# Kernel tuning notes

Measured on AMD Instinct MI355X. Metric: run time of the kernel, lower is better.

## Reference

```python
import jax, jax.numpy as jnp
import numpy as np

# dims
N, D, H = 10000, 512, 8            # nodes, node hidden, heads
E, EL, M = 120000, 60000, 600000   # graph edges, local edges, line-graph edges
ED, EH = 64, 8                     # edge feat dim (relation_share_heads), edge heads
L, R = 4, 100                      # gnn layers, relation vocab
DK, EDK = D // H, ED // EH
SCALE_N, SCALE_E = float(np.sqrt(DK)), float(np.sqrt(EDK))


def layer_norm(h, g, b, eps=1e-5):
    mu = jnp.mean(h, axis=-1, keepdims=True)
    var = jnp.mean((h - mu) ** 2, axis=-1, keepdims=True)
    return (h - mu) * jax.lax.rsqrt(var + eps) * g + b


def setup_inputs() -> dict:
    key = jax.random.key(0)
    ks = iter(jax.random.split(key, 80))

    def nrm(shape, s=0.02):
        return jax.random.normal(next(ks), shape, jnp.float32) * s

    inp = {
        "x": jax.random.normal(next(ks), (N, D), jnp.float32),
        "rel_embed": nrm((R, ED), 1.0),
        # node-update (RAT) params, stacked over layers
        "Wq": nrm((L, D, D)), "bq": jnp.zeros((L, D), jnp.float32),
        "Wk": nrm((L, D, D)), "Wv": nrm((L, D, D)),
        "Wo": nrm((L, D, D)), "bo": jnp.zeros((L, D), jnp.float32),
        "ln1_g": jnp.ones((L, D), jnp.float32), "ln1_b": jnp.zeros((L, D), jnp.float32),
        "F1": nrm((L, D, 4 * D)), "f1b": jnp.zeros((L, 4 * D), jnp.float32),
        "F2": nrm((L, 4 * D, D)), "f2b": jnp.zeros((L, D), jnp.float32),
        "ln2_g": jnp.ones((L, D), jnp.float32), "ln2_b": jnp.zeros((L, D), jnp.float32),
        # edge-update (metapath line-graph attention) params
        "Eq": nrm((L, ED, ED)), "eqb": jnp.zeros((L, ED), jnp.float32),
        "Ek": nrm((L, ED, ED)), "Ev": nrm((L, ED, ED)),
        "Eo": nrm((L, ED, ED)), "eob": jnp.zeros((L, ED), jnp.float32),
        "Ns": nrm((L, D, ED)), "nsb": jnp.zeros((L, ED), jnp.float32),
        "Nd": nrm((L, D, ED)), "ndb": jnp.zeros((L, ED), jnp.float32),
        "eln1_g": jnp.ones((L, ED), jnp.float32), "eln1_b": jnp.zeros((L, ED), jnp.float32),
        "G1": nrm((L, ED, 4 * ED)), "g1b": jnp.zeros((L, 4 * ED), jnp.float32),
        "G2": nrm((L, 4 * ED, ED)), "g2b": jnp.zeros((L, ED), jnp.float32),
        "eln2_g": jnp.ones((L, ED), jnp.float32), "eln2_b": jnp.zeros((L, ED), jnp.float32),
        # graph structure (constants)
        "edge_feat": jax.random.randint(next(ks), (E,), 0, R),
        "local_index": jnp.arange(EL),
        "src_ids": jax.random.randint(next(ks), (EL,), 0, N),
        "dst_ids": jax.random.randint(next(ks), (EL,), 0, N),
        "g_src": jax.random.randint(next(ks), (E,), 0, N),
        "g_dst": jax.random.randint(next(ks), (E,), 0, N),
        "lg_src": jax.random.randint(next(ks), (M,), 0, EL),
        "lg_dst": jax.random.randint(next(ks), (M,), 0, EL),
    }
    return inp


def reference(x, rel_embed, Wq, bq, Wk, Wv, Wo, bo, ln1_g, ln1_b, F1, f1b, F2, f2b,
              ln2_g, ln2_b, Eq, eqb, Ek, Ev, Eo, eob, Ns, nsb, Nd, ndb,
              eln1_g, eln1_b, G1, g1b, G2, g2b, eln2_g, eln2_b,
              edge_feat, local_index, src_ids, dst_ids, g_src, g_dst, lg_src, lg_dst):
    lg_x = rel_embed[edge_feat]        # [E, ED] relation embedding gather
    lg_x_local = lg_x[local_index]     # [EL, ED]
    for i in range(L):
        x_in = x
        # ---- node update: relation-aware multi-head attention over g ----
        q = (x_in @ Wq[i] + bq[i]).reshape(N, H, DK)
        k = (x_in @ Wk[i]).reshape(N, H, DK)
        v = (x_in @ Wv[i]).reshape(N, H, DK)
        e = lg_x[:, None, :]           # relation feat shared across heads (edim == d_k)
        ks = k[g_src] + e              # [E, H, DK]
        vs = v[g_src] + e
        s = jnp.einsum('ehd,ehd->eh', ks, q[g_dst]) / SCALE_N
        w = jnp.exp(jnp.clip(s, -10.0, 10.0))
        wv = jax.ops.segment_sum(w[..., None] * vs, g_dst, num_segments=N)
        z = jax.ops.segment_sum(w, g_dst, num_segments=N)
        o = (wv / jnp.maximum(z, 1e-9)[..., None]).reshape(N, D)
        h = layer_norm(x_in + o @ Wo[i] + bo[i], ln1_g[i], ln1_b[i])
        x = layer_norm(h + jax.nn.relu(h @ F1[i] + f1b[i]) @ F2[i] + f2b[i], ln2_g[i], ln2_b[i])
        # ---- edge update: attention over line graph lg, metapath = shared node feat ----
        src_x = x_in[src_ids]          # index_select on pre-update x
        dst_x = x_in[dst_ids]
        qe = (lg_x_local @ Eq[i] + eqb[i] + src_x @ Ns[i] + nsb[i]).reshape(EL, EH, EDK)
        me = (dst_x @ Nd[i] + ndb[i]).reshape(EL, EH, EDK)
        ke = (lg_x_local @ Ek[i]).reshape(EL, EH, EDK) + me
        ve = (lg_x_local @ Ev[i]).reshape(EL, EH, EDK) + me
        se = jnp.einsum('mhd,mhd->mh', ke[lg_src], qe[lg_dst]) / SCALE_E
        we = jnp.exp(jnp.clip(se, -10.0, 10.0))
        wve = jax.ops.segment_sum(we[..., None] * ve[lg_src], lg_dst, num_segments=EL)
        ze = jax.ops.segment_sum(we, lg_dst, num_segments=EL)
        oe = (wve / jnp.maximum(ze, 1e-9)[..., None]).reshape(EL, ED)
        he = layer_norm(lg_x_local + oe @ Eo[i] + eob[i], eln1_g[i], eln1_b[i])
        out_local = layer_norm(he + jax.nn.relu(he @ G1[i] + g1b[i]) @ G2[i] + g2b[i],
                               eln2_g[i], eln2_b[i])
        lg_x = lg_x.at[local_index].set(out_local)   # masked_scatter_
        lg_x_local = out_local
    return (x, lg_x_local)
```

## Files before the change

kernel.cpp:

```cpp
#include <hip/hip_runtime.h>
#include <math.h>

#define NN   10000
#define DD   512
#define NH   8
#define NE   120000
#define NEL  60000
#define NLG  600000
#define ED   64
#define NEH  8
#define NL   4
#define QKVW 1536

typedef __attribute__((ext_vector_type(8))) short bf16x8;
typedef __attribute__((ext_vector_type(8))) unsigned short u16x8;
typedef __attribute__((ext_vector_type(4))) float f32x4;

__device__ __forceinline__ unsigned short f2b(float f) {
    union { float f; unsigned u; } c; c.f = f;
    unsigned u = c.u;
    unsigned r = u + 0x7FFFu + ((u >> 16) & 1u);
    return (unsigned short)(r >> 16);
}
__device__ __forceinline__ float b2f(unsigned short b) {
// ... 88 lines not shown

static __global__ __launch_bounds__(256)
void hist2_k(const int* __restrict__ gdst, const int* __restrict__ ldst,
             int* __restrict__ gcnt, int* __restrict__ ecnt) {
    int i = blockIdx.x * 256 + threadIdx.x;
    if (i < NE) atomicAdd(&gcnt[gdst[i]], 1);
    else if (i < NE + NLG) atomicAdd(&ecnt[ldst[i - NE]], 1);
}

static __global__ __launch_bounds__(256)
void scanA2_k(const int* __restrict__ gcnt, const int* __restrict__ ecnt,
              int* __restrict__ goff, int* __restrict__ eoff,
              int* __restrict__ bsum, int nbG) {
    __shared__ int sm[256];
    const int t = threadIdx.x;
    const bool isG = blockIdx.x < (unsigned)nbG;
    const int b = isG ? blockIdx.x : blockIdx.x - nbG;
    const int n = isG ? NN : NEL;
    const int* cnt = isG ? gcnt : ecnt;
    int* off = isG ? goff : eoff;
    int* bs = bsum + (isG ? 0 : 512);
    const int i = b * 256 + t;
    int v = (i < n) ? cnt[i] : 0;
    sm[t] = v; __syncthreads();
    int x = v;
    #pragma unroll
    for (int d = 1; d < 256; d <<= 1) {
        int y = (t >= d) ? sm[t - d] : 0;
        __syncthreads();
        x += y; sm[t] = x; __syncthreads();
    }
    if (i < n) off[i] = x - v;
    if (t == 255) bs[b] = x;
}

static __global__ __launch_bounds__(1024)
void scanB2_k(int* __restrict__ bsum, int nbG, int nbE) {
    __shared__ int sm[1024];
    const int t = threadIdx.x;
    int* bs = bsum + (blockIdx.x ? 512 : 0);
    const int nb = blockIdx.x ? nbE : nbG;
    int v = (t < nb) ? bs[t] : 0;
    sm[t] = v; __syncthreads();
    int x = v;
    #pragma unroll
    for (int d = 1; d < 1024; d <<= 1) {
        int y = (t >= d) ? sm[t - d] : 0;
        __syncthreads();
        x += y; sm[t] = x; __syncthreads();
    }
    if (t < nb) bs[t] = x - v;
}

static __global__ __launch_bounds__(256)
void scanC2_k(const int* __restrict__ bsum, int* __restrict__ goff,
              int* __restrict__ eoff, int* __restrict__ gcur,
              int* __restrict__ ecur, int nbG) {
    const bool isG = blockIdx.x < (unsigned)nbG;
    const int b = isG ? blockIdx.x : blockIdx.x - nbG;
    const int n = isG ? NN : NEL;
    int* off = isG ? goff : eoff;
    int* cur = isG ? gcur : ecur;
    const int* bs = bsum + (isG ? 0 : 512);
    int i = b * 256 + threadIdx.x;
    if (i < n) { int o = off[i] + bs[b]; off[i] = o; cur[i] = o; }
}

static __global__ __launch_bounds__(256)
void scatterpack_k(const int* __restrict__ gdst, const int* __restrict__ ldst,
                   const int* __restrict__ gsrc, const int* __restrict__ lsrc,
                   int* __restrict__ gcur, int* __restrict__ ecur,
                   int2* __restrict__ npack, int* __restrict__ esrc) {
    int i = blockIdx.x * 256 + threadIdx.x;
    if (i < NE) {
        int p = atomicAdd(&gcur[gdst[i]], 1);
        npack[p] = make_int2(i, gsrc[i]);
    } else if (i < NE + NLG) {
        int k = i - NE;
        int p = atomicAdd(&ecur[ldst[k]], 1);
        esrc[p] = lsrc[k];
    }
}

static __global__ __launch_bounds__(256)
void gemm_bf16_k(const unsigned short* __restrict__ A,
                 const unsigned short* __restrict__ A2, const int* __restrict__ idx2,
                 const unsigned short* __restrict__ Bt, const float* __restrict__ bias,
                 const float* __restrict__ addC, const unsigned short* __restrict__ addCb,
                 float* __restrict__ C, unsigned short* __restrict__ Cb,
                 int M, int K, int Nc, int doRelu, int K1)
{
    __shared__ unsigned short Asl[64 * 64];
    __shared__ unsigned short Bsl[64 * 64];
    const int tid  = threadIdx.x;
    const int lane = tid & 63;
    const int wave = tid >> 6;
    const int wr = (wave >> 1) * 32;
    const int wc = (wave & 1) * 32;

    const int nwg = gridDim.x * gridDim.y;
    const int hw = blockIdx.y * gridDim.x + blockIdx.x;
    const int q8 = nwg >> 3, r8 = nwg & 7;
    const int xcd = hw & 7, rest = hw >> 3;
    const int logical = (xcd < r8 ? xcd * (q8 + 1) : r8 * (q8 + 1) + (xcd - r8) * q8) + rest;
    const int bm = (logical / gridDim.x) * 64;
    const int bn = (logical % gridDim.x) * 64;

    const int rl8 = lane >> 3;
    const int sl8 = lane & 7;
    int ga[2]; long ia[2]; bool av[2]; int acw[2];
    int gb[2]; int bcw[2];
    #pragma unroll
    for (int c = 0; c < 2; ++c) {
        int ar = wave * 16 + c * 8 + rl8;
        ga[c] = bm + ar;
        av[c] = ga[c] < M;
        ia[c] = (A2 && av[c]) ? (long)idx2[ga[c]] : 0;
        acw[c] = (sl8 ^ (ar & 7)) * 8;
        int br = wave * 16 + c * 8 + rl8;
        gb[c] = bn + br;
        bcw[c] = (sl8 ^ (br & 7)) * 8;
    }

    auto stage = [&](int k0) {
        #pragma unroll
        for (int c = 0; c < 2; ++c) {
            const unsigned short* s;
            if (!A2)            s = A  + (long)ga[c] * K  + k0 + acw[c];
            else if (k0 < K1)   s = A  + (long)ga[c] * K1 + k0 + acw[c];
            else                s = A2 + ia[c] * DD + (k0 - K1) + acw[c];
            if (av[c]) gl16(s, Asl + (wave * 16 + c * 8) * 64);
            gl16(Bt + (long)gb[c] * K + k0 + bcw[c], Bsl + (wave * 16 + c * 8) * 64);
        }
    };

    f32x4 acc[2][2] = {};
    const int rbase = lane & 15;
    const int ks = lane >> 4;

    for (int k0 = 0; k0 < K; k0 += 64) {
        stage(k0);
        __syncthreads();
        #pragma unroll
        for (int h = 0; h < 2; ++h) {
            bf16x8 af[2], bfr[2];
            #pragma unroll
            for (int mi = 0; mi < 2; ++mi) {
                int r = wr + mi * 16 + rbase;
                int p = (h * 4 + ks) ^ (r & 7);
                af[mi] = *reinterpret_cast<const bf16x8*>(Asl + r * 64 + p * 8);
            }
            #pragma unroll
            for (int ni = 0; ni < 2; ++ni) {
                int r = wc + ni * 16 + rbase;
                int p = (h * 4 + ks) ^ (r & 7);
                bfr[ni] = *reinterpret_cast<const bf16x8*>(Bsl + r * 64 + p * 8);
            }
            #pragma unroll
            for (int mi = 0; mi < 2; ++mi)
                #pragma unroll
                for (int ni = 0; ni < 2; ++ni)
                    acc[mi][ni] = __builtin_amdgcn_mfma_f32_16x16x32_bf16(
                        af[mi], bfr[ni], acc[mi][ni], 0, 0, 0);
        }
        __syncthreads();
    }

    const int colBase = bn + wc + rbase;
    const int rowBase = bm + wr + ks * 4;
    #pragma unroll
    for (int mi = 0; mi < 2; ++mi) {
        #pragma unroll
        for (int j = 0; j < 4; ++j) {
            int r = rowBase + mi * 16 + j;
            if (r >= M) continue;
            long ro = (long)r * Nc;
            #pragma unroll
            for (int ni = 0; ni < 2; ++ni) {
                int cc = colBase + ni * 16;
                if (cc >= Nc) continue;
                float v = acc[mi][ni][j];
                if (bias)  v += bias[cc];
                if (doRelu) v = fmaxf(v, 0.0f);
                if (addC)  v += addC[ro + cc];
                else if (addCb) v += b2f(addCb[ro + cc]);
                if (Cb) Cb[ro + cc] = f2b(v);
                else    C[ro + cc] = v;
            }
        }
    }
}

static __global__ __launch_bounds__(256)
void ln_k(const float* __restrict__ in, const unsigned short* __restrict__ inb,
          const float* __restrict__ g, const float* __restrict__ b,
          float* __restrict__ out, int Dw, int nrows,
          unsigned short* __restrict__ outb,
          unsigned short* __restrict__ out2b, const int* __restrict__ idx2)
{
    const int row = blockIdx.x * 4 + (threadIdx.x >> 6);
    if (row >= nrows) return;
    const int lane = threadIdx.x & 63;
    const int per = Dw >> 6;
    float v[8];
    float s = 0.f;
    if (inb) {
        const unsigned short* rp = inb + (long)row * Dw;
        for (int i = 0; i < per; ++i) { v[i] = b2f(rp[i * 64 + lane]); s += v[i]; }
    } else {
        const float* rp = in + (long)row * Dw;
        for (int i = 0; i < per; ++i) { v[i] = rp[i * 64 + lane]; s += v[i]; }
    }
    #pragma unroll
    for (int off = 32; off; off >>= 1) s += __shfl_xor(s, off, 64);
    const float mu = s / (float)Dw;
    float var = 0.f;
    for (int i = 0; i < per; ++i) { float d = v[i] - mu; var += d * d; }
    #pragma unroll
    for (int off = 32; off; off >>= 1) var += __shfl_xor(var, off, 64);
    const float rstd = rsqrtf(var / (float)Dw + 1e-5f);
    for (int i = 0; i < per; ++i) {
        int c = i * 64 + lane;
        float o = (v[i] - mu) * rstd * g[c] + b[c];
        if (out)   out[(long)row * Dw + c] = o;
        if (outb)  outb[(long)row * Dw + c] = f2b(o);
        if (out2b) out2b[(long)idx2[row] * Dw + c] = f2b(o);
    }
}

static __global__ __launch_bounds__(256)
void node_attn_csr_k(const unsigned short* __restrict__ qkv,
                     const unsigned short* __restrict__ lgb,
                     const int* __restrict__ goff, const int2* __restrict__ npack,
                     unsigned short* __restrict__ ob)
{
    int node = blockIdx.x * 4 + (threadIdx.x >> 6);
    if (node >= NN) return;
    const int lane = threadIdx.x & 63;
    float qv[8];
    {
        u16x8 q8 = *reinterpret_cast<const u16x8*>(qkv + (long)node * QKVW + lane * 8);
        #pragma unroll
        for (int i = 0; i < 8; ++i) qv[i] = b2f(q8[i]);
    }
    float wva[8] = {0.f, 0.f, 0.f, 0.f, 0.f, 0.f, 0.f, 0.f};
    float zac = 0.f;
    int j = goff[node];
    const int hi = (node + 1 < NN) ? goff[node + 1] : NE;
    const int eoffl = (lane & 7) * 8;

    for (; j + 2 <= hi; j += 2) {
        int2 pa = npack[j], pb = npack[j + 1];
        u16x8 kA = *reinterpret_cast<const u16x8*>(qkv + (long)pa.y * QKVW + 512 + lane * 8);
        u16x8 vA = *reinterpret_cast<const u16x8*>(qkv + (long)pa.y * QKVW + 1024 + lane * 8);
        u16x8 eA = *reinterpret_cast<const u16x8*>(lgb + (long)pa.x * ED + eoffl);
        u16x8 kB = *reinterpret_cast<const u16x8*>(qkv + (long)pb.y * QKVW + 512 + lane * 8);
        u16x8 vB = *reinterpret_cast<const u16x8*>(qkv + (long)pb.y * QKVW + 1024 + lane * 8);
        u16x8 eB = *reinterpret_cast<const u16x8*>(lgb + (long)pb.x * ED + eoffl);
        float edA[8], vvA[8], edB[8], vvB[8];
        float pA = 0.f, pB = 0.f;
        #pragma unroll
        for (int i = 0; i < 8; ++i) {
            edA[i] = b2f(eA[i]); vvA[i] = b2f(vA[i]);
            pA = fmaf(b2f(kA[i]) + edA[i], qv[i], pA);
            edB[i] = b2f(eB[i]); vvB[i] = b2f(vB[i]);
            pB = fmaf(b2f(kB[i]) + edB[i], qv[i], pB);
        }
        pA += __shfl_xor(pA, 1, 64); pA += __shfl_xor(pA, 2, 64); pA += __shfl_xor(pA, 4, 64);
        pB += __shfl_xor(pB, 1, 64); pB += __shfl_xor(pB, 2, 64); pB += __shfl_xor(pB, 4, 64);
        float wA = expf(fminf(fmaxf(pA * 0.125f, -10.0f), 10.0f));
        float wB = expf(fminf(fmaxf(pB * 0.125f, -10.0f), 10.0f));
        #pragma unroll
        for (int i = 0; i < 8; ++i) {
            wva[i] = fmaf(wA, vvA[i] + edA[i], wva[i]);
            wva[i] = fmaf(wB, vvB[i] + edB[i], wva[i]);
        }
        zac += wA + wB;
    }
    for (; j < hi; ++j) {
        int2 pa = npack[j];
        u16x8 kA = *reinterpret_cast<const u16x8*>(qkv + (long)pa.y * QKVW + 512 + lane * 8);
        u16x8 vA = *reinterpret_cast<const u16x8*>(qkv + (long)pa.y * QKVW + 1024 + lane * 8);
        u16x8 eA = *reinterpret_cast<const u16x8*>(lgb + (long)pa.x * ED + eoffl);
        float edA[8], vvA[8];
        float pA = 0.f;
        #pragma unroll
        for (int i = 0; i < 8; ++i) {
            edA[i] = b2f(eA[i]); vvA[i] = b2f(vA[i]);
            pA = fmaf(b2f(kA[i]) + edA[i], qv[i], pA);
        }
        pA += __shfl_xor(pA, 1, 64); pA += __shfl_xor(pA, 2, 64); pA += __shfl_xor(pA, 4, 64);
        float wA = expf(fminf(fmaxf(pA * 0.125f, -10.0f), 10.0f));
        #pragma unroll
        for (int i = 0; i < 8; ++i) wva[i] = fmaf(wA, vvA[i] + edA[i], wva[i]);
        zac += wA;
    }
    const float inv = 1.0f / fmaxf(zac, 1e-9f);
    u16x8 o8;
    #pragma unroll
    for (int i = 0; i < 8; ++i) o8[i] = f2b(wva[i] * inv);
    *reinterpret_cast<u16x8*>(ob + (long)node * DD + lane * 8) = o8;
}

static __global__ __launch_bounds__(256)
void lg_attn_csr_k(const unsigned short* __restrict__ qeb,
                   const unsigned short* __restrict__ keve,
                   const int* __restrict__ eoff, const int* __restrict__ esrc,
                   unsigned short* __restrict__ oeb)
{
    int d = blockIdx.x * 4 + (threadIdx.x >> 6);
    if (d >= NEL) return;
    const int lane = threadIdx.x & 63;
    const int he = lane & 7;
    const int ee = lane >> 3;
    const int hd = lane >> 3;
    float qv8[8];
    {
        u16x8 q8 = *reinterpret_cast<const u16x8*>(qeb + (long)d * ED + he * 8);
        #pragma unroll
        for (int i = 0; i < 8; ++i) qv8[i] = b2f(q8[i]);
    }
    const float qvd = b2f(qeb[(long)d * ED + lane]);
    float oa = 0.f, zac = 0.f;
    int j = eoff[d];
    const int hi = (d + 1 < NEL) ? eoff[d + 1] : NLG;

    for (; j + 8 <= hi; j += 8) {
        int sMine = esrc[j + ee];
        u16x8 k8 = *reinterpret_cast<const u16x8*>(keve + (long)sMine * 128 + he * 8);
        float p = 0.f;
        #pragma unroll
        for (int i = 0; i < 8; ++i) p = fmaf(b2f(k8[i]), qv8[i], p);
        float w = expf(fminf(fmaxf(p * 0.35355339059327373f, -10.0f), 10.0f));
        #pragma unroll
        for (int u = 0; u < 8; ++u) {
            float wu = __shfl(w, u * 8 + hd, 64);
            int   su = esrc[j + u];
            float vv = b2f(keve[(long)su * 128 + 64 + lane]);
            oa = fmaf(wu, vv, oa);
            zac += wu;
        }
    }
    for (; j < hi; ++j) {
        int s = esrc[j];
        float kv = b2f(keve[(long)s * 128 + lane]);
        float vv = b2f(keve[(long)s * 128 + 64 + lane]);
        float p = kv * qvd;
        p += __shfl_xor(p, 1, 64); p += __shfl_xor(p, 2, 64); p += __shfl_xor(p, 4, 64);
        float w = expf(fminf(fmaxf(p * 0.35355339059327373f, -10.0f), 10.0f));
        oa = fmaf(w, vv, oa);
        zac += w;
    }
    oeb[(long)d * ED + lane] = f2b(oa / fmaxf(zac, 1e-9f));
}

static inline void run_gemm(hipStream_t st, const unsigned short* A,
                            const unsigned short* Bt, const float* bias,
                            const float* addC, const unsigned short* addCb,
                            float* C, unsigned short* Cb,
                            int M, int K, int Nc, int relu)
{
    dim3 g((Nc + 63) / 64, (M + 63) / 64);
    gemm_bf16_k<<<g, 256, 0, st>>>(A, nullptr, nullptr, Bt, bias, addC, addCb,
                                   C, Cb, M, K, Nc, relu, 0);
}
static inline void run_gemm2(hipStream_t st, const unsigned short* A1,
                             const unsigned short* A2, const int* idx2,
                             const unsigned short* Bt, const float* bias,
                             unsigned short* Cb, int M, int K, int Nc, int K1)
{
    dim3 g((Nc + 63) / 64, (M + 63) / 64);
    gemm_bf16_k<<<g, 256, 0, st>>>(A1, A2, idx2, Bt, bias, nullptr, nullptr,
                                   nullptr, Cb, M, K, Nc, 0, K1);
}

extern "C" void kernel_launch(void* const* d_in, const int* in_sizes, int n_in,
                              void* d_out, int out_size, void* d_ws, size_t ws_size,
                              hipStream_t stream)
{
    const float* x_in  = (const float*)d_in[0];
    const float* rel   = (const float*)d_in[1];
    const float* Wq    = (const float*)d_in[2];
    const float* bq    = (const float*)d_in[3];
    const float* Wk    = (const float*)d_in[4];
    const float* Wv    = (const float*)d_in[5];
    const float* Wo    = (const float*)d_in[6];
    const float* bo    = (const float*)d_in[7];
    const float* ln1g  = (const float*)d_in[8];
    const float* ln1b  = (const float*)d_in[9];
    const float* F1    = (const float*)d_in[10];
    const float* f1b   = (const float*)d_in[11];
    const float* F2    = (const float*)d_in[12];
    const float* f2b_  = (const float*)d_in[13];
    const float* ln2g  = (const float*)d_in[14];
    const float* ln2b  = (const float*)d_in[15];
    const float* Eq    = (const float*)d_in[16];
    const float* eqb   = (const float*)d_in[17];
    const float* Ek    = (const float*)d_in[18];
    const float* Ev    = (const float*)d_in[19];
    const float* Eo    = (const float*)d_in[20];
    const float* eob   = (const float*)d_in[21];
    const float* Ns    = (const float*)d_in[22];
    const float* nsb   = (const float*)d_in[23];
    const float* Nd    = (const float*)d_in[24];
    const float* ndb   = (const float*)d_in[25];
    const float* eln1g = (const float*)d_in[26];
    const float* eln1b = (const float*)d_in[27];
    const float* G1    = (const float*)d_in[28];
    const float* g1b   = (const float*)d_in[29];
    const float* G2    = (const float*)d_in[30];
    const float* g2b   = (const float*)d_in[31];
    const float* eln2g = (const float*)d_in[32];
    const float* eln2b = (const float*)d_in[33];
    const int* edge_feat   = (const int*)d_in[34];
    const int* local_index = (const int*)d_in[35];
    const int* src_ids     = (const int*)d_in[36];
    const int* dst_ids     = (const int*)d_in[37];
    const int* g_src       = (const int*)d_in[38];
    const int* g_dst       = (const int*)d_in[39];
    const int* lg_src      = (const int*)d_in[40];
    const int* lg_dst      = (const int*)d_in[41];

    float* xbuf = (float*)d_out;
    float* el   = xbuf + (size_t)NN * DD;

    float* W = (float*)d_ws;
    size_t off = 0;
    auto alloc = [&](size_t n) { float* p = W + off; off += (n + 63) & ~(size_t)63; return p; };
    float* qkvb = alloc((size_t)NL * QKVW);
    float* kvb  = alloc((size_t)NL * 128);
    float* qb2  = alloc((size_t)NL * ED);

    unsigned short* bp = (unsigned short*)(W + off);
    size_t boff = 0;
    auto balloc = [&](size_t n) { unsigned short* p = bp + boff; boff += (n + 63) & ~(size_t)63; return p; };
    unsigned short* lgb = balloc((size_t)NE * ED);
    unsigned short* xb  = balloc((size_t)NN * DD);
    unsigned short* qkv = balloc((size_t)NN * QKVW);
    unsigned short* elb = balloc((size_t)NEL * ED);
    unsigned short* e1b = balloc((size_t)NEL * ED);
    unsigned short* heb = balloc((size_t)NEL * ED);
    unsigned short* qeb = balloc((size_t)NEL * ED);
    unsigned short* fgb = balloc((size_t)NN * 4 * DD);
    unsigned short* t0b = balloc((size_t)NN * DD);
    unsigned short* t2b = balloc((size_t)NEL * ED);
    unsigned short* t3b = balloc((size_t)NEL * ED);
    unsigned short* xpb = balloc((size_t)NN * DD);
    unsigned short* hb   = qkv;
    unsigned short* keve = qkv + (size_t)NN * DD;
    unsigned short* ob   = fgb;
    unsigned short* WqkvT = balloc((size_t)NL * QKVW * DD);
    unsigned short* WoT  = balloc((size_t)NL * DD * DD);
    unsigned short* F1T  = balloc((size_t)NL * DD * 4 * DD);
    unsigned short* F2T  = balloc((size_t)NL * 4 * DD * DD);
    unsigned short* KVET = balloc((size_t)NL * 128 * 576);
    unsigned short* QET  = balloc((size_t)NL * 64 * 576);
    unsigned short* EoT  = balloc((size_t)NL * ED * ED);
    unsigned short* G1T  = balloc((size_t)NL * ED * 4 * ED);
    unsigned short* G2T  = balloc((size_t)NL * 4 * ED * ED);
    int* ip = (int*)(bp + ((boff + 63) & ~(size_t)63));
    size_t ioff = 0;
    auto ialloc = [&](size_t n) { int* p = ip + ioff; ioff += (n + 63) & ~(size_t)63; return p; };
    int* gcnt = ialloc(NN);
    int* goff = ialloc(NN);
    int* gcur = ialloc(NN);
    int2* npack = (int2*)ialloc(2 * (size_t)NE);
    int* ecnt = ialloc(NEL);
    int* eoff = ialloc(NEL);
    int* ecur = ialloc(NEL);
    int* esrc = ialloc(NLG);
    int* bsum = ialloc(1024);

    TT tt;
    int bc = 0, si = 0;
    auto seg = [&](const float* src, unsigned short* dst, int K, int N,
                   long lstride, int rowStride, int rowOff, int colOff) {
        tt.src[si] = src; tt.dst[si] = dst; tt.lstride[si] = lstride;
        tt.K[si] = K; tt.Nn[si] = N; tt.rowStride[si] = rowStride;
        tt.rowOff[si] = rowOff; tt.colOff[si] = colOff;
        tt.blkStart[si] = bc;
        bc += (K / 32) * (N / 32) * NL;
        ++si;
    };
    seg(Wq, WqkvT, 512, 512, (long)QKVW * DD, DD, 0, 0);
    seg(Wk, WqkvT, 512, 512, (long)QKVW * DD, DD, 512, 0);
    seg(Wv, WqkvT, 512, 512, (long)QKVW * DD, DD, 1024, 0);
    seg(Wo, WoT, 512, 512, (long)DD * DD, DD, 0, 0);
    seg(F1, F1T, 512, 2048, (long)DD * 4 * DD, DD, 0, 0);
    seg(F2, F2T, 2048, 512, (long)4 * DD * DD, 4 * DD, 0, 0);
    seg(Ek, KVET, 64, 64, (long)128 * 576, 576, 0, 0);
    seg(Nd, KVET, 512, 64, (long)128 * 576, 576, 0, 64);
    seg(Ev, KVET, 64, 64, (long)128 * 576, 576, 64, 0);
    seg(Nd, KVET, 512, 64, (long)128 * 576, 576, 64, 64);
    seg(Eq, QET, 64, 64, (long)64 * 576, 576, 0, 0);
    seg(Ns, QET, 512, 64, (long)64 * 576, 576, 0, 64);
    seg(Eo, EoT, 64, 64, (long)ED * ED, ED, 0, 0);
    seg(G1, G1T, 64, 256, (long)ED * 4 * ED, ED, 0, 0);
    seg(G2, G2T, 256, 64, (long)4 * ED * ED, 4 * ED, 0, 0);
    ttrans_all_k<<<bc, 256, 0, stream>>>(tt);
    biases_k<<<(NL * QKVW + 255) / 256, 256, 0, stream>>>(bq, ndb, eqb, nsb, qkvb, kvb, qb2);

    const int nbG = (NN + 255) / 256, nbE = (NEL + 255) / 256;
    zero2_k<<<nbE, 256, 0, stream>>>(gcnt, ecnt);
    hist2_k<<<(NE + NLG + 255) / 256, 256, 0, stream>>>(g_dst, lg_dst, gcnt, ecnt);
    scanA2_k<<<nbG + nbE, 256, 0, stream>>>(gcnt, ecnt, goff, eoff, bsum, nbG);
    scanB2_k<<<2, 1024, 0, stream>>>(bsum, nbG, nbE);
    scanC2_k<<<nbG + nbE, 256, 0, stream>>>(bsum, goff, eoff, gcur, ecur, nbG);
    scatterpack_k<<<(NE + NLG + 255) / 256, 256, 0, stream>>>(
        g_dst, lg_dst, g_src, lg_src, gcur, ecur, npack, esrc);

    {
        long tot = (long)NN * DD + (long)NE * ED + (long)NEL * ED;
        init_all_k<<<(int)((tot + 255) / 256), 256, 0, stream>>>(
            x_in, rel, edge_feat, local_index, xbuf, xb, lgb, el, elb);
    }

    for (int i = 0; i < NL; ++i) {
        size_t oD2 = (size_t)i * DD * DD, oE2 = (size_t)i * ED * ED;

        run_gemm(stream, xb, WqkvT + (size_t)i * QKVW * DD, qkvb + (size_t)i * QKVW,
                 nullptr, nullptr, nullptr, qkv, NN, DD, QKVW, 0);
        node_attn_csr_k<<<NN / 4, 256, 0, stream>>>(qkv, lgb, goff, npack, ob);
        run_gemm(stream, ob, WoT + oD2, bo + (size_t)i * DD, nullptr, xb, nullptr, t0b, NN, DD, DD, 0);
        ln_k<<<(NN + 3) / 4, 256, 0, stream>>>(nullptr, t0b, ln1g + (size_t)i * DD, ln1b + (size_t)i * DD,
                                               nullptr, DD, NN, hb, nullptr, nullptr);

        run_gemm2(stream, elb, xb, dst_ids, KVET + (size_t)i * 128 * 576,
                  kvb + (size_t)i * 128, keve, NEL, 576, 128, 64);
        run_gemm2(stream, elb, xb, src_ids, QET + (size_t)i * 64 * 576,
                  qb2 + (size_t)i * 64, qeb, NEL, 576, 64, 64);
        lg_attn_csr_k<<<NEL / 4, 256, 0, stream>>>(qeb, keve, eoff, esrc, e1b);
        run_gemm(stream, e1b, EoT + oE2, eob + (size_t)i * ED, nullptr, elb, nullptr, t2b, NEL, ED, ED, 0);
        ln_k<<<(NEL + 3) / 4, 256, 0, stream>>>(nullptr, t2b, eln1g + (size_t)i * ED, eln1b + (size_t)i * ED,
                                                nullptr, ED, NEL, heb, nullptr, nullptr);
        run_gemm(stream, heb, G1T + (size_t)i * ED * 4 * ED, g1b + (size_t)i * 4 * ED,
                 nullptr, nullptr, nullptr, fgb, NEL, ED, 4 * ED, 1);
        run_gemm(stream, fgb, G2T + (size_t)i * 4 * ED * ED, g2b + (size_t)i * ED,
                 nullptr, heb, nullptr, t3b, NEL, 4 * ED, ED, 0);
        ln_k<<<(NEL + 3) / 4, 256, 0, stream>>>(nullptr, t3b, eln2g + (size_t)i * ED, eln2b + (size_t)i * ED,
                                                el, ED, NEL, elb, lgb, local_index);

        run_gemm(stream, hb, F1T + (size_t)i * DD * 4 * DD, f1b + (size_t)i * 4 * DD,
                 nullptr, nullptr, nullptr, fgb, NN, DD, 4 * DD, 1);
        run_gemm(stream, fgb, F2T + (size_t)i * 4 * DD * DD, f2b_ + (size_t)i * DD,
                 nullptr, hb, nullptr, xpb, NN, 2048, DD, 0);
        ln_k<<<(NN + 3) / 4, 256, 0, stream>>>(nullptr, xpb, ln2g + (size_t)i * DD, ln2b + (size_t)i * DD,
                                               xbuf, DD, NN, xb, nullptr, nullptr);
    }
}
```

Measured before the change: 1.625 ms.

## Batch independent node and edge GEMMs into grouped segmented launches

Adds a segmented GEMM kernel that takes up to three independent problem descriptors and maps a single flat grid across them. The node QKV projection and the two edge projection GEMMs now share one launch, and so do the node output and edge output projections. The two attention kernels are moved next to each other. keve gets its own buffer so it no longer aliases qkv. The aim is to fill the GPU better with the small edge GEMMs and to cut launch gaps, at the cost of extra register pressure and per-block segment lookup.

```diff
diff --git a/kernel.cpp b/kernel.cpp
--- a/kernel.cpp
+++ b/kernel.cpp
@@ -194,13 +194,20 @@
     }
 }
 
-static __global__ __launch_bounds__(256)
-void gemm_bf16_k(const unsigned short* __restrict__ A,
-                 const unsigned short* __restrict__ A2, const int* __restrict__ idx2,
-                 const unsigned short* __restrict__ Bt, const float* __restrict__ bias,
-                 const float* __restrict__ addC, const unsigned short* __restrict__ addCb,
-                 float* __restrict__ C, unsigned short* __restrict__ Cb,
-                 int M, int K, int Nc, int doRelu, int K1)
+struct GSeg {
+    const unsigned short* A;
+    const unsigned short* A2;
+    const int* idx2;
+    const unsigned short* Bt;
+    const float* bias;
+    const unsigned short* addCb;
+    unsigned short* Cb;
+    int M, K, Nc, K1, blkStart, gridX;
+};
+struct GSegs { GSeg s[3]; int nseg; int total; };
+
+static __global__ __launch_bounds__(256)
+void gemmseg_k(GSegs g)
 {
     __shared__ unsigned short Asl[64 * 64];
     __shared__ unsigned short Bsl[64 * 64];
@@ -210,13 +217,20 @@
     const int wr = (wave >> 1) * 32;
     const int wc = (wave & 1) * 32;
 
-    const int nwg = gridDim.x * gridDim.y;
-    const int hw = blockIdx.y * gridDim.x + blockIdx.x;
+    const int nwg = g.total;
+    const int hw = blockIdx.x;
     const int q8 = nwg >> 3, r8 = nwg & 7;
     const int xcd = hw & 7, rest = hw >> 3;
     const int logical = (xcd < r8 ? xcd * (q8 + 1) : r8 * (q8 + 1) + (xcd - r8) * q8) + rest;
-    const int bm = (logical / gridDim.x) * 64;
-    const int bn = (logical % gridDim.x) * 64;
+
+    int si = 0;
+    #pragma unroll
+    for (int i = 1; i < 3; ++i) si += (i < g.nseg && logical >= g.s[i].blkStart);
+    const GSeg S = g.s[si];
+    const int local = logical - S.blkStart;
+    const int bm = (local / S.gridX) * 64;
+    const int bn = (local % S.gridX) * 64;
+    const int M = S.M, K = S.K, Nc = S.Nc, K1 = S.K1;
 
     const int rl8 = lane >> 3;
     const int sl8 = lane & 7;
@@ -227,7 +241,7 @@
         int ar = wave * 16 + c * 8 + rl8;
         ga[c] = bm + ar;
         av[c] = ga[c] < M;
-        ia[c] = (A2 && av[c]) ? (long)idx2[ga[c]] : 0;
+        ia[c] = (S.A2 && av[c]) ? (long)S.idx2[ga[c]] : 0;
         acw[c] = (sl8 ^ (ar & 7)) * 8;
         int br = wave * 16 + c * 8 + rl8;
         gb[c] = bn + br;
@@ -238,11 +252,11 @@
         #pragma unroll
         for (int c = 0; c < 2; ++c) {
             const unsigned short* s;
-            if (!A2)            s = A  + (long)ga[c] * K  + k0 + acw[c];
-            else if (k0 < K1)   s = A  + (long)ga[c] * K1 + k0 + acw[c];
-            else                s = A2 + ia[c] * DD + (k0 - K1) + acw[c];
+            if (!S.A2)          s = S.A  + (long)ga[c] * K  + k0 + acw[c];
+            else if (k0 < K1)   s = S.A  + (long)ga[c] * K1 + k0 + acw[c];
+            else                s = S.A2 + ia[c] * DD + (k0 - K1) + acw[c];
             if (av[c]) gl16(s, Asl + (wave * 16 + c * 8) * 64);
-            gl16(Bt + (long)gb[c] * K + k0 + bcw[c], Bsl + (wave * 16 + c * 8) * 64);
+            gl16(S.Bt + (long)gb[c] * K + k0 + bcw[c], Bsl + (wave * 16 + c * 8) * 64);
         }
     };
 
@@ -292,6 +306,112 @@
                 int cc = colBase + ni * 16;
                 if (cc >= Nc) continue;
                 float v = acc[mi][ni][j];
+                if (S.bias)  v += S.bias[cc];
+                if (S.addCb) v += b2f(S.addCb[ro + cc]);
+                S.Cb[ro + cc] = f2b(v);
+            }
+        }
+    }
+}
+
+static __global__ __launch_bounds__(256)
+void gemm_bf16_k(const unsigned short* __restrict__ A,
+                 const unsigned short* __restrict__ A2, const int* __restrict__ idx2,
+                 const unsigned short* __restrict__ Bt, const float* __restrict__ bias,
+                 const float* __restrict__ addC, const unsigned short* __restrict__ addCb,
+                 float* __restrict__ C, unsigned short* __restrict__ Cb,
+                 int M, int K, int Nc, int doRelu, int K1)
+{
+    __shared__ unsigned short Asl[64 * 64];
+    __shared__ unsigned short Bsl[64 * 64];
+    const int tid  = threadIdx.x;
+    const int lane = tid & 63;
+    const int wave = tid >> 6;
+    const int wr = (wave >> 1) * 32;
+    const int wc = (wave & 1) * 32;
+
+    const int nwg = gridDim.x * gridDim.y;
+    const int hw = blockIdx.y * gridDim.x + blockIdx.x;
+    const int q8 = nwg >> 3, r8 = nwg & 7;
+    const int xcd = hw & 7, rest = hw >> 3;
+    const int logical = (xcd < r8 ? xcd * (q8 + 1) : r8 * (q8 + 1) + (xcd - r8) * q8) + rest;
+    const int bm = (logical / gridDim.x) * 64;
+    const int bn = (logical % gridDim.x) * 64;
+
+    const int rl8 = lane >> 3;
+    const int sl8 = lane & 7;
+    int ga[2]; long ia[2]; bool av[2]; int acw[2];
+    int gb[2]; int bcw[2];
+    #pragma unroll
+    for (int c = 0; c < 2; ++c) {
+        int ar = wave * 16 + c * 8 + rl8;
+        ga[c] = bm + ar;
+        av[c] = ga[c] < M;
+        ia[c] = (A2 && av[c]) ? (long)idx2[ga[c]] : 0;
+        acw[c] = (sl8 ^ (ar & 7)) * 8;
+        int br = wave * 16 + c * 8 + rl8;
+        gb[c] = bn + br;
+        bcw[c] = (sl8 ^ (br & 7)) * 8;
+    }
+
+    auto stage = [&](int k0) {
+        #pragma unroll
+        for (int c = 0; c < 2; ++c) {
+            const unsigned short* s;
+            if (!A2)            s = A  + (long)ga[c] * K  + k0 + acw[c];
+            else if (k0 < K1)   s = A  + (long)ga[c] * K1 + k0 + acw[c];
+            else                s = A2 + ia[c] * DD + (k0 - K1) + acw[c];
+            if (av[c]) gl16(s, Asl + (wave * 16 + c * 8) * 64);
+            gl16(Bt + (long)gb[c] * K + k0 + bcw[c], Bsl + (wave * 16 + c * 8) * 64);
+        }
+    };
+
+    f32x4 acc[2][2] = {};
+    const int rbase = lane & 15;
+    const int ks = lane >> 4;
+
+    for (int k0 = 0; k0 < K; k0 += 64) {
+        stage(k0);
+        __syncthreads();
+        #pragma unroll
+        for (int h = 0; h < 2; ++h) {
+            bf16x8 af[2], bfr[2];
+            #pragma unroll
+            for (int mi = 0; mi < 2; ++mi) {
+                int r = wr + mi * 16 + rbase;
+                int p = (h * 4 + ks) ^ (r & 7);
+                af[mi] = *reinterpret_cast<const bf16x8*>(Asl + r * 64 + p * 8);
+            }
+            #pragma unroll
+            for (int ni = 0; ni < 2; ++ni) {
+                int r = wc + ni * 16 + rbase;
+                int p = (h * 4 + ks) ^ (r & 7);
+                bfr[ni] = *reinterpret_cast<const bf16x8*>(Bsl + r * 64 + p * 8);
+            }
+            #pragma unroll
+            for (int mi = 0; mi < 2; ++mi)
+                #pragma unroll
+                for (int ni = 0; ni < 2; ++ni)
+                    acc[mi][ni] = __builtin_amdgcn_mfma_f32_16x16x32_bf16(
+                        af[mi], bfr[ni], acc[mi][ni], 0, 0, 0);
+        }
+        __syncthreads();
+    }
+
+    const int colBase = bn + wc + rbase;
+    const int rowBase = bm + wr + ks * 4;
+    #pragma unroll
+    for (int mi = 0; mi < 2; ++mi) {
+        #pragma unroll
+        for (int j = 0; j < 4; ++j) {
+            int r = rowBase + mi * 16 + j;
+            if (r >= M) continue;
+            long ro = (long)r * Nc;
+            #pragma unroll
+            for (int ni = 0; ni < 2; ++ni) {
+                int cc = colBase + ni * 16;
+                if (cc >= Nc) continue;
+                float v = acc[mi][ni][j];
                 if (bias)  v += bias[cc];
                 if (doRelu) v = fmaxf(v, 0.0f);
                 if (addC)  v += addC[ro + cc];
@@ -475,15 +595,6 @@
     dim3 g((Nc + 63) / 64, (M + 63) / 64);
     gemm_bf16_k<<<g, 256, 0, st>>>(A, nullptr, nullptr, Bt, bias, addC, addCb,
                                    C, Cb, M, K, Nc, relu, 0);
-}
-static inline void run_gemm2(hipStream_t st, const unsigned short* A1,
-                             const unsigned short* A2, const int* idx2,
-                             const unsigned short* Bt, const float* bias,
-                             unsigned short* Cb, int M, int K, int Nc, int K1)
-{
-    dim3 g((Nc + 63) / 64, (M + 63) / 64);
-    gemm_bf16_k<<<g, 256, 0, st>>>(A1, A2, idx2, Bt, bias, nullptr, nullptr,
-                                   nullptr, Cb, M, K, Nc, 0, K1);
 }
 
 extern "C" void kernel_launch(void* const* d_in, const int* in_sizes, int n_in,
@@ -549,6 +660,7 @@
     unsigned short* lgb = balloc((size_t)NE * ED);
     unsigned short* xb  = balloc((size_t)NN * DD);
     unsigned short* qkv = balloc((size_t)NN * QKVW);
+    unsigned short* keve = balloc((size_t)NEL * 128);
     unsigned short* elb = balloc((size_t)NEL * ED);
     unsigned short* e1b = balloc((size_t)NEL * ED);
     unsigned short* heb = balloc((size_t)NEL * ED);
@@ -559,7 +671,6 @@
     unsigned short* t3b = balloc((size_t)NEL * ED);
     unsigned short* xpb = balloc((size_t)NN * DD);
     unsigned short* hb   = qkv;
-    unsigned short* keve = qkv + (size_t)NN * DD;
     unsigned short* ob   = fgb;
     unsigned short* WqkvT = balloc((size_t)NL * QKVW * DD);
     unsigned short* WoT  = balloc((size_t)NL * DD * DD);
@@ -627,24 +738,51 @@
             x_in, rel, edge_feat, local_index, xbuf, xb, lgb, el, elb);
     }
 
+    const int rQ = (NN + 63) / 64;
+    const int rE = (NEL + 63) / 64;
+
     for (int i = 0; i < NL; ++i) {
         size_t oD2 = (size_t)i * DD * DD, oE2 = (size_t)i * ED * ED;
 
-        run_gemm(stream, xb, WqkvT + (size_t)i * QKVW * DD, qkvb + (size_t)i * QKVW,
-                 nullptr, nullptr, nullptr, qkv, NN, DD, QKVW, 0);
+        {
+            GSegs G;
+            G.s[0] = { xb, nullptr, nullptr, WqkvT + (size_t)i * QKVW * DD,
+                       qkvb + (size_t)i * QKVW, nullptr, qkv,
+                       NN, DD, QKVW, 0, 0, QKVW / 64 };
+            int b0 = (QKVW / 64) * rQ;
+            G.s[1] = { elb, xb, dst_ids, KVET + (size_t)i * 128 * 576,
+                       kvb + (size_t)i * 128, nullptr, keve,
+                       NEL, 576, 128, 64, b0, 2 };
+            int b1 = b0 + 2 * rE;
+            G.s[2] = { elb, xb, src_ids, QET + (size_t)i * 64 * 576,
+                       qb2 + (size_t)i * 64, nullptr, qeb,
+                       NEL, 576, 64, 64, b1, 1 };
+            G.nseg = 3; G.total = b1 + rE;
+            gemmseg_k<<<G.total, 256, 0, stream>>>(G);
+        }
+
         node_attn_csr_k<<<NN / 4, 256, 0, stream>>>(qkv, lgb, goff, npack, ob);
-        run_gemm(stream, ob, WoT + oD2, bo + (size_t)i * DD, nullptr, xb, nullptr, t0b, NN, DD, DD, 0);
+        lg_attn_csr_k<<<NEL / 4, 256, 0, stream>>>(qeb, keve, eoff, esrc, e1b);
+
+        {
+            GSegs G;
+            G.s[0] = { ob, nullptr, nullptr, WoT + oD2,
+                       bo + (size_t)i * DD, xb, t0b,
+                       NN, DD, DD, 0, 0, DD / 64 };
+            int b0 = (DD / 64) * rQ;
+            G.s[1] = { e1b, nullptr, nullptr, EoT + oE2,
+                       eob + (size_t)i * ED, elb, t2b,
+                       NEL, ED, ED, 0, b0, 1 };
+            G.s[2] = G.s[1];
+            G.nseg = 2; G.total = b0 + rE;
+            gemmseg_k<<<G.total, 256, 0, stream>>>(G);
+        }
+
         ln_k<<<(NN + 3) / 4, 256, 0, stream>>>(nullptr, t0b, ln1g + (size_t)i * DD, ln1b + (size_t)i * DD,
                                                nullptr, DD, NN, hb, nullptr, nullptr);
-
-        run_gemm2(stream, elb, xb, dst_ids, KVET + (size_t)i * 128 * 576,
-                  kvb + (size_t)i * 128, keve, NEL, 576, 128, 64);
-        run_gemm2(stream, elb, xb, src_ids, QET + (size_t)i * 64 * 576,
-                  qb2 + (size_t)i * 64, qeb, NEL, 576, 64, 64);
-        lg_attn_csr_k<<<NEL / 4, 256, 0, stream>>>(qeb, keve, eoff, esrc, e1b);
-        run_gemm(stream, e1b, EoT + oE2, eob + (size_t)i * ED, nullptr, elb, nullptr, t2b, NEL, ED, ED, 0);
         ln_k<<<(NEL + 3) / 4, 256, 0, stream>>>(nullptr, t2b, eln1g + (size_t)i * ED, eln1b + (size_t)i * ED,
                                                 nullptr, ED, NEL, heb, nullptr, nullptr);
+
         run_gemm(stream, heb, G1T + (size_t)i * ED * 4 * ED, g1b + (size_t)i * 4 * ED,
                  nullptr, nullptr, nullptr, fgb, NEL, ED, 4 * ED, 1);
         run_gemm(stream, fgb, G2T + (size_t)i * 4 * ED * ED, g2b + (size_t)i * ED,
```

Measured after the change: 1.576 ms (median of 2 runs). 3.0% less time.

## Batch independent node and edge GEMMs, attention and layernorms into grouped launches

Applied to the files above, without the earlier changes.

Replaces separate per-op launches with segmented grouped kernels. Independent node-path and edge-path work (QKV plus edge KV/Q GEMMs, both attention passes, both output projections, paired layernorms, and paired FFN GEMMs) now runs in a single launch per stage. This cuts kernel launch count and tail underutilization by letting small edge GEMMs fill the GPU alongside node GEMMs. The cost is extra buffers to avoid aliasing, such as a separate keve, plus per-block segment selection and reuse of keve as the edge FFN scratch.

```diff
diff --git a/kernel.cpp b/kernel.cpp
--- a/kernel.cpp
+++ b/kernel.cpp
@@ -194,13 +194,20 @@
     }
 }
 
-static __global__ __launch_bounds__(256)
-void gemm_bf16_k(const unsigned short* __restrict__ A,
-                 const unsigned short* __restrict__ A2, const int* __restrict__ idx2,
-                 const unsigned short* __restrict__ Bt, const float* __restrict__ bias,
-                 const float* __restrict__ addC, const unsigned short* __restrict__ addCb,
-                 float* __restrict__ C, unsigned short* __restrict__ Cb,
-                 int M, int K, int Nc, int doRelu, int K1)
+struct GSeg {
+    const unsigned short* A;
+    const unsigned short* A2;
+    const int* idx2;
+    const unsigned short* Bt;
+    const float* bias;
+    const unsigned short* addCb;
+    unsigned short* Cb;
+    int M, K, Nc, K1, blkStart, gridX, doRelu;
+};
+struct GSegs { GSeg s[3]; int nseg; int total; };
+
+static __global__ __launch_bounds__(256)
+void gemmseg_k(GSegs g)
 {
     __shared__ unsigned short Asl[64 * 64];
     __shared__ unsigned short Bsl[64 * 64];
@@ -210,13 +217,20 @@
     const int wr = (wave >> 1) * 32;
     const int wc = (wave & 1) * 32;
 
-    const int nwg = gridDim.x * gridDim.y;
-    const int hw = blockIdx.y * gridDim.x + blockIdx.x;
+    const int nwg = g.total;
+    const int hw = blockIdx.x;
     const int q8 = nwg >> 3, r8 = nwg & 7;
     const int xcd = hw & 7, rest = hw >> 3;
     const int logical = (xcd < r8 ? xcd * (q8 + 1) : r8 * (q8 + 1) + (xcd - r8) * q8) + rest;
-    const int bm = (logical / gridDim.x) * 64;
-    const int bn = (logical % gridDim.x) * 64;
+
+    int si = 0;
+    #pragma unroll
+    for (int i = 1; i < 3; ++i) si += (i < g.nseg && logical >= g.s[i].blkStart);
+    const GSeg S = g.s[si];
+    const int local = logical - S.blkStart;
+    const int bm = (local / S.gridX) * 64;
+    const int bn = (local % S.gridX) * 64;
+    const int M = S.M, K = S.K, Nc = S.Nc, K1 = S.K1;
 
     const int rl8 = lane >> 3;
     const int sl8 = lane & 7;
@@ -227,7 +241,7 @@
         int ar = wave * 16 + c * 8 + rl8;
         ga[c] = bm + ar;
         av[c] = ga[c] < M;
-        ia[c] = (A2 && av[c]) ? (long)idx2[ga[c]] : 0;
+        ia[c] = (S.A2 && av[c]) ? (long)S.idx2[ga[c]] : 0;
         acw[c] = (sl8 ^ (ar & 7)) * 8;
         int br = wave * 16 + c * 8 + rl8;
         gb[c] = bn + br;
@@ -238,11 +252,11 @@
         #pragma unroll
         for (int c = 0; c < 2; ++c) {
             const unsigned short* s;
-            if (!A2)            s = A  + (long)ga[c] * K  + k0 + acw[c];
-            else if (k0 < K1)   s = A  + (long)ga[c] * K1 + k0 + acw[c];
-            else                s = A2 + ia[c] * DD + (k0 - K1) + acw[c];
+            if (!S.A2)          s = S.A  + (long)ga[c] * K  + k0 + acw[c];
+            else if (k0 < K1)   s = S.A  + (long)ga[c] * K1 + k0 + acw[c];
+            else                s = S.A2 + ia[c] * DD + (k0 - K1) + acw[c];
             if (av[c]) gl16(s, Asl + (wave * 16 + c * 8) * 64);
-            gl16(Bt + (long)gb[c] * K + k0 + bcw[c], Bsl + (wave * 16 + c * 8) * 64);
+            gl16(S.Bt + (long)gb[c] * K + k0 + bcw[c], Bsl + (wave * 16 + c * 8) * 64);
         }
     };
 
@@ -292,63 +306,61 @@
                 int cc = colBase + ni * 16;
                 if (cc >= Nc) continue;
                 float v = acc[mi][ni][j];
-                if (bias)  v += bias[cc];
-                if (doRelu) v = fmaxf(v, 0.0f);
-                if (addC)  v += addC[ro + cc];
-                else if (addCb) v += b2f(addCb[ro + cc]);
-                if (Cb) Cb[ro + cc] = f2b(v);
-                else    C[ro + cc] = v;
+                if (S.bias)  v += S.bias[cc];
+                if (S.doRelu) v = fmaxf(v, 0.0f);
+                if (S.addCb) v += b2f(S.addCb[ro + cc]);
+                S.Cb[ro + cc] = f2b(v);
             }
         }
     }
 }
 
-static __global__ __launch_bounds__(256)
-void ln_k(const float* __restrict__ in, const unsigned short* __restrict__ inb,
-          const float* __restrict__ g, const float* __restrict__ b,
-          float* __restrict__ out, int Dw, int nrows,
-          unsigned short* __restrict__ outb,
-          unsigned short* __restrict__ out2b, const int* __restrict__ idx2)
+struct LNSeg {
+    const unsigned short* inb;
+    const float* g; const float* b;
+    float* out;
+    unsigned short* outb;
+    unsigned short* out2b;
+    const int* idx2;
+    int Dw, nrows, blkStart;
+};
+struct LNSegs { LNSeg s[2]; };
+
+static __global__ __launch_bounds__(256)
+void ln2_k(LNSegs L)
 {
-    const int row = blockIdx.x * 4 + (threadIdx.x >> 6);
-    if (row >= nrows) return;
+    const int sidx = (blockIdx.x >= (unsigned)L.s[1].blkStart) ? 1 : 0;
+    const LNSeg S = L.s[sidx];
+    const int row = (blockIdx.x - S.blkStart) * 4 + (threadIdx.x >> 6);
+    if (row >= S.nrows) return;
     const int lane = threadIdx.x & 63;
-    const int per = Dw >> 6;
+    const int per = S.Dw >> 6;
     float v[8];
     float s = 0.f;
-    if (inb) {
-        const unsigned short* rp = inb + (long)row * Dw;
-        for (int i = 0; i < per; ++i) { v[i] = b2f(rp[i * 64 + lane]); s += v[i]; }
-    } else {
-        const float* rp = in + (long)row * Dw;
-        for (int i = 0; i < per; ++i) { v[i] = rp[i * 64 + lane]; s += v[i]; }
-    }
+    const unsigned short* rp = S.inb + (long)row * S.Dw;
+    for (int i = 0; i < per; ++i) { v[i] = b2f(rp[i * 64 + lane]); s += v[i]; }
     #pragma unroll
     for (int off = 32; off; off >>= 1) s += __shfl_xor(s, off, 64);
-    const float mu = s / (float)Dw;
+    const float mu = s / (float)S.Dw;
     float var = 0.f;
     for (int i = 0; i < per; ++i) { float d = v[i] - mu; var += d * d; }
     #pragma unroll
     for (int off = 32; off; off >>= 1) var += __shfl_xor(var, off, 64);
-    const float rstd = rsqrtf(var / (float)Dw + 1e-5f);
+    const float rstd = rsqrtf(var / (float)S.Dw + 1e-5f);
     for (int i = 0; i < per; ++i) {
         int c = i * 64 + lane;
-        float o = (v[i] - mu) * rstd * g[c] + b[c];
-        if (out)   out[(long)row * Dw + c] = o;
-        if (outb)  outb[(long)row * Dw + c] = f2b(o);
-        if (out2b) out2b[(long)idx2[row] * Dw + c] = f2b(o);
-    }
-}
-
-static __global__ __launch_bounds__(256)
-void node_attn_csr_k(const unsigned short* __restrict__ qkv,
-                     const unsigned short* __restrict__ lgb,
-                     const int* __restrict__ goff, const int2* __restrict__ npack,
-                     unsigned short* __restrict__ ob)
+        float o = (v[i] - mu) * rstd * S.g[c] + S.b[c];
+        if (S.out)   S.out[(long)row * S.Dw + c] = o;
+        if (S.outb)  S.outb[(long)row * S.Dw + c] = f2b(o);
+        if (S.out2b) S.out2b[(long)S.idx2[row] * S.Dw + c] = f2b(o);
+    }
+}
+
+__device__ __forceinline__ void node_attn_body(
+    const unsigned short* __restrict__ qkv, const unsigned short* __restrict__ lgb,
+    const int* __restrict__ goff, const int2* __restrict__ npack,
+    unsigned short* __restrict__ ob, int node, int lane)
 {
-    int node = blockIdx.x * 4 + (threadIdx.x >> 6);
-    if (node >= NN) return;
-    const int lane = threadIdx.x & 63;
     float qv[8];
     {
         u16x8 q8 = *reinterpret_cast<const u16x8*>(qkv + (long)node * QKVW + lane * 8);
@@ -414,15 +426,11 @@
     *reinterpret_cast<u16x8*>(ob + (long)node * DD + lane * 8) = o8;
 }
 
-static __global__ __launch_bounds__(256)
-void lg_attn_csr_k(const unsigned short* __restrict__ qeb,
-                   const unsigned short* __restrict__ keve,
-                   const int* __restrict__ eoff, const int* __restrict__ esrc,
-                   unsigned short* __restrict__ oeb)
+__device__ __forceinline__ void lg_attn_body(
+    const unsigned short* __restrict__ qeb, const unsigned short* __restrict__ keve,
+    const int* __restrict__ eoff, const int* __restrict__ esrc,
+    unsigned short* __restrict__ oeb, int d, int lane)
 {
-    int d = blockIdx.x * 4 + (threadIdx.x >> 6);
-    if (d >= NEL) return;
-    const int lane = threadIdx.x & 63;
     const int he = lane & 7;
     const int ee = lane >> 3;
     const int hd = lane >> 3;
@@ -466,24 +474,25 @@
     oeb[(long)d * ED + lane] = f2b(oa / fmaxf(zac, 1e-9f));
 }
 
-static inline void run_gemm(hipStream_t st, const unsigned short* A,
-                            const unsigned short* Bt, const float* bias,
-                            const float* addC, const unsigned short* addCb,
-                            float* C, unsigned short* Cb,
-                            int M, int K, int Nc, int relu)
+static __global__ __launch_bounds__(256)
+void attn_both_k(const unsigned short* __restrict__ qkv,
+                 const unsigned short* __restrict__ lgb,
+                 const int* __restrict__ goff, const int2* __restrict__ npack,
+                 unsigned short* __restrict__ ob,
+                 const unsigned short* __restrict__ qeb,
+                 const unsigned short* __restrict__ keve,
+                 const int* __restrict__ eoff, const int* __restrict__ esrc,
+                 unsigned short* __restrict__ oeb)
 {
-    dim3 g((Nc + 63) / 64, (M + 63) / 64);
-    gemm_bf16_k<<<g, 256, 0, st>>>(A, nullptr, nullptr, Bt, bias, addC, addCb,
-                                   C, Cb, M, K, Nc, relu, 0);
-}
-static inline void run_gemm2(hipStream_t st, const unsigned short* A1,
-                             const unsigned short* A2, const int* idx2,
-                             const unsigned short* Bt, const float* bias,
-                             unsigned short* Cb, int M, int K, int Nc, int K1)
-{
-    dim3 g((Nc + 63) / 64, (M + 63) / 64);
-    gemm_bf16_k<<<g, 256, 0, st>>>(A1, A2, idx2, Bt, bias, nullptr, nullptr,
-                                   nullptr, Cb, M, K, Nc, 0, K1);
+    const int lane = threadIdx.x & 63;
+    const int wv = threadIdx.x >> 6;
+    if (blockIdx.x < NN / 4) {
+        int node = blockIdx.x * 4 + wv;
+        node_attn_body(qkv, lgb, goff, npack, ob, node, lane);
+    } else {
+        int d = (blockIdx.x - NN / 4) * 4 + wv;
+        if (d < NEL) lg_attn_body(qeb, keve, eoff, esrc, oeb, d, lane);
+    }
 }
 
 extern "C" void kernel_launch(void* const* d_in, const int* in_sizes, int n_in,
@@ -549,17 +558,18 @@
     unsigned short* lgb = balloc((size_t)NE * ED);
     unsigned short* xb  = balloc((size_t)NN * DD);
     unsigned short* qkv = balloc((size_t)NN * QKVW);
+    unsigned short* keve = balloc((size_t)NEL * 128);
+    unsigned short* qeb  = balloc((size_t)NEL * ED);
+    unsigned short* t0b  = balloc((size_t)NN * DD);
+    unsigned short* gfe  = keve;
     unsigned short* elb = balloc((size_t)NEL * ED);
     unsigned short* e1b = balloc((size_t)NEL * ED);
     unsigned short* heb = balloc((size_t)NEL * ED);
-    unsigned short* qeb = balloc((size_t)NEL * ED);
     unsigned short* fgb = balloc((size_t)NN * 4 * DD);
-    unsigned short* t0b = balloc((size_t)NN * DD);
     unsigned short* t2b = balloc((size_t)NEL * ED);
     unsigned short* t3b = balloc((size_t)NEL * ED);
     unsigned short* xpb = balloc((size_t)NN * DD);
     unsigned short* hb   = qkv;
-    unsigned short* keve = qkv + (size_t)NN * DD;
     unsigned short* ob   = fgb;
     unsigned short* WqkvT = balloc((size_t)NL * QKVW * DD);
     unsigned short* WoT  = balloc((size_t)NL * DD * DD);
@@ -627,36 +637,90 @@
             x_in, rel, edge_feat, local_index, xbuf, xb, lgb, el, elb);
     }
 
+    const int rQ = (NN + 63) / 64;
+    const int rE = (NEL + 63) / 64;
+
     for (int i = 0; i < NL; ++i) {
         size_t oD2 = (size_t)i * DD * DD, oE2 = (size_t)i * ED * ED;
 
-        run_gemm(stream, xb, WqkvT + (size_t)i * QKVW * DD, qkvb + (size_t)i * QKVW,
-                 nullptr, nullptr, nullptr, qkv, NN, DD, QKVW, 0);
-        node_attn_csr_k<<<NN / 4, 256, 0, stream>>>(qkv, lgb, goff, npack, ob);
-        run_gemm(stream, ob, WoT + oD2, bo + (size_t)i * DD, nullptr, xb, nullptr, t0b, NN, DD, DD, 0);
-        ln_k<<<(NN + 3) / 4, 256, 0, stream>>>(nullptr, t0b, ln1g + (size_t)i * DD, ln1b + (size_t)i * DD,
-                                               nullptr, DD, NN, hb, nullptr, nullptr);
-
-        run_gemm2(stream, elb, xb, dst_ids, KVET + (size_t)i * 128 * 576,
-                  kvb + (size_t)i * 128, keve, NEL, 576, 128, 64);
-        run_gemm2(stream, elb, xb, src_ids, QET + (size_t)i * 64 * 576,
-                  qb2 + (size_t)i * 64, qeb, NEL, 576, 64, 64);
-        lg_attn_csr_k<<<NEL / 4, 256, 0, stream>>>(qeb, keve, eoff, esrc, e1b);
-        run_gemm(stream, e1b, EoT + oE2, eob + (size_t)i * ED, nullptr, elb, nullptr, t2b, NEL, ED, ED, 0);
-        ln_k<<<(NEL + 3) / 4, 256, 0, stream>>>(nullptr, t2b, eln1g + (size_t)i * ED, eln1b + (size_t)i * ED,
-                                                nullptr, ED, NEL, heb, nullptr, nullptr);
-        run_gemm(stream, heb, G1T + (size_t)i * ED * 4 * ED, g1b + (size_t)i * 4 * ED,
-                 nullptr, nullptr, nullptr, fgb, NEL, ED, 4 * ED, 1);
-        run_gemm(stream, fgb, G2T + (size_t)i * 4 * ED * ED, g2b + (size_t)i * ED,
-                 nullptr, heb, nullptr, t3b, NEL, 4 * ED, ED, 0);
-        ln_k<<<(NEL + 3) / 4, 256, 0, stream>>>(nullptr, t3b, eln2g + (size_t)i * ED, eln2b + (size_t)i * ED,
-                                                el, ED, NEL, elb, lgb, local_index);
-
-        run_gemm(stream, hb, F1T + (size_t)i * DD * 4 * DD, f1b + (size_t)i * 4 * DD,
-                 nullptr, nullptr, nullptr, fgb, NN, DD, 4 * DD, 1);
-        run_gemm(stream, fgb, F2T + (size_t)i * 4 * DD * DD, f2b_ + (size_t)i * DD,
-                 nullptr, hb, nullptr, xpb, NN, 2048, DD, 0);
-        ln_k<<<(NN + 3) / 4, 256, 0, stream>>>(nullptr, xpb, ln2g + (size_t)i * DD, ln2b + (size_t)i * DD,
-                                               xbuf, DD, NN, xb, nullptr, nullptr);
-    }
-}
+        {
+            GSegs G;
+            G.s[0] = { xb, nullptr, nullptr, WqkvT + (size_t)i * QKVW * DD,
+                       qkvb + (size_t)i * QKVW, nullptr, qkv,
+                       NN, DD, QKVW, 0, 0, QKVW / 64, 0 };
+            int b0 = (QKVW / 64) * rQ;
+            G.s[1] = { elb, xb, dst_ids, KVET + (size_t)i * 128 * 576,
+                       kvb + (size_t)i * 128, nullptr, keve,
+                       NEL, 576, 128, 64, b0, 2, 0 };
+            int b1 = b0 + 2 * rE;
+            G.s[2] = { elb, xb, src_ids, QET + (size_t)i * 64 * 576,
+                       qb2 + (size_t)i * 64, nullptr, qeb,
+                       NEL, 576, 64, 64, b1, 1, 0 };
+            G.nseg = 3; G.total = b1 + rE;
+            gemmseg_k<<<G.total, 256, 0, stream>>>(G);
+        }
+
+        attn_both_k<<<NN / 4 + (NEL + 3) / 4, 256, 0, stream>>>(
+            qkv, lgb, goff, npack, ob, qeb, keve, eoff, esrc, e1b);
+
+        {
+            GSegs G;
+            G.s[0] = { ob, nullptr, nullptr, WoT + oD2,
+                       bo + (size_t)i * DD, xb, t0b,
+                       NN, DD, DD, 0, 0, DD / 64, 0 };
+            int b0 = (DD / 64) * rQ;
+            G.s[1] = { e1b, nullptr, nullptr, EoT + oE2,
+                       eob + (size_t)i * ED, elb, t2b,
+                       NEL, ED, ED, 0, b0, 1, 0 };
+            G.s[2] = G.s[1];
+            G.nseg = 2; G.total = b0 + rE;
+            gemmseg_k<<<G.total, 256, 0, stream>>>(G);
+        }
+
+        {
+            LNSegs L;
+            L.s[0] = { t0b, ln1g + (size_t)i * DD, ln1b + (size_t)i * DD,
+                       nullptr, hb, nullptr, nullptr, DD, NN, 0 };
+            L.s[1] = { t2b, eln1g + (size_t)i * ED, eln1b + (size_t)i * ED,
+                       nullptr, heb, nullptr, nullptr, ED, NEL, (NN + 3) / 4 };
+            ln2_k<<<(NN + 3) / 4 + (NEL + 3) / 4, 256, 0, stream>>>(L);
+        }
+
+        {
+            GSegs G;
+            G.s[0] = { heb, nullptr, nullptr, G1T + (size_t)i * ED * 4 * ED,
+                       g1b + (size_t)i * 4 * ED, nullptr, gfe,
+                       NEL, ED, 4 * ED, 0, 0, (4 * ED) / 64, 1 };
+            int b0 = ((4 * ED) / 64) * rE;
+            G.s[1] = { hb, nullptr, nullptr, F1T + (size_t)i * DD * 4 * DD,
+                       f1b + (size_t)i * 4 * DD, nullptr, fgb,
+                       NN, DD, 4 * DD, 0, b0, (4 * DD) / 64, 1 };
+            G.s[2] = G.s[1];
+            G.nseg = 2; G.total = b0 + ((4 * DD) / 64) * rQ;
+            gemmseg_k<<<G.total, 256, 0, stream>>>(G);
+        }
+
+        {
+            GSegs G;
+            G.s[0] = { gfe, nullptr, nullptr, G2T + (size_t)i * 4 * ED * ED,
+                       g2b + (size_t)i * ED, heb, t3b,
+                       NEL, 4 * ED, ED, 0, 0, 1, 0 };
+            int b0 = rE;
+            G.s[1] = { fgb, nullptr, nullptr, F2T + (size_t)i * 4 * DD * DD,
+                       f2b_ + (size_t)i * DD, hb, xpb,
+                       NN, 4 * DD, DD, 0, b0, DD / 64, 0 };
+            G.s[2] = G.s[1];
+            G.nseg = 2; G.total = b0 + (DD / 64) * rQ;
+            gemmseg_k<<<G.total, 256, 0, stream>>>(G);
+        }
+
+        {
+            LNSegs L;
+            L.s[0] = { t3b, eln2g + (size_t)i * ED, eln2b + (size_t)i * ED,
+                       el, elb, lgb, local_index, ED, NEL, 0 };
+            L.s[1] = { xpb, ln2g + (size_t)i * DD, ln2b + (size_t)i * DD,
+                       xbuf, xb, nullptr, nullptr, DD, NN, (NEL + 3) / 4 };
+            ln2_k<<<(NEL + 3) / 4 + (NN + 3) / 4, 256, 0, stream>>>(L);
+        }
+    }
+}
```

After: 1.669 ms. 2.7% more time.
